# Kernel optimization log

Hardware: AMD Instinct MI355X
Metric: run time of the kernel (lower is better)

The kernel has to match this reference:

```python
import jax, jax.numpy as jnp
import numpy as np

# dims
B, T, E = 2, 4096, 512
H = 8
DH = E // H            # 64 per-head dim
DEPTH = 4
NHASH = 4              # n_hashes
BUCKET = 64            # bucket_size
NB = T // BUCKET       # n_buckets = 64 (even)
VOCAB, NCLASS = 32000, 10
FF = 4 * E
MASK_VAL = -1e9        # causal mask value
SELF_VAL = -5e4        # TOKEN_SELF_ATTN_VALUE


def layer_norm(x, g, b):
    m = jnp.mean(x, axis=-1, keepdims=True)
    v = jnp.var(x, axis=-1, keepdims=True)
    return (x - m) * jax.lax.rsqrt(v + 1e-5) * g + b


def lsh_attention(x, wqk, wv, wo, bo, rot):
    """Reformer LSH causal self-attention (eval mode, shared QK, n_hashes rounds)."""
    qk = (x @ wqk).reshape(B, T, H, DH).transpose(0, 2, 1, 3).reshape(B * H, T, DH)
    v = (x @ wv).reshape(B, T, H, DH).transpose(0, 2, 1, 3).reshape(B * H, T, DH)
    b = B * H
    # --- hash: random rotations -> bucket ids per hash round ---
    rotated = jnp.einsum('btf,fhi->bhti', qk, rot)             # (b, NHASH, T, NB//2)
    rotated = jnp.concatenate([rotated, -rotated], axis=-1)    # (b, NHASH, T, NB)
    buckets = jnp.argmax(rotated, axis=-1)                     # (b, NHASH, T)
    buckets = buckets + (jnp.arange(NHASH) * NB)[None, :, None]
    buckets = buckets.reshape(b, NHASH * T)
    # --- stable sort by (bucket, time) ---
    ticker = jnp.arange(NHASH * T)
    bt = buckets * T + (ticker % T)
    sticker = jnp.argsort(bt, axis=-1)                         # sort permutation
    undo_sort = jnp.argsort(sticker, axis=-1)
    st = sticker % T                                           # original time index of sorted slot
    sqk = jnp.take_along_axis(qk, st[..., None], axis=1)
    sv = jnp.take_along_axis(v, st[..., None], axis=1)
    # --- chunk into buckets, attend to own + previous chunk ---
    C = NHASH * NB                                             # number of chunks
    bq_t = st.reshape(b, C, BUCKET)
    bqk = sqk.reshape(b, C, BUCKET, DH)
    bv = sv.reshape(b, C, BUCKET, DH)
    bq = bqk
    bk = bqk / jnp.maximum(jnp.linalg.norm(bqk, axis=-1, keepdims=True), 1e-12)
    look = lambda t: jnp.concatenate([t, jnp.roll(t, 1, axis=1)], axis=2)
    bk, bvl, bkv_t = look(bk), look(bv), look(bq_t)
    dots = jnp.einsum('bcie,bcje->bcij', bq, bk) * (DH ** -0.5)  # (b, C, BUCKET, 2*BUCKET)
    causal = bq_t[:, :, :, None] < bkv_t[:, :, None, :]
    dots = jnp.where(causal, MASK_VAL, dots)
    self_m = bq_t[:, :, :, None] == bkv_t[:, :, None, :]
    dots = jnp.where(self_m, SELF_VAL, dots)
    lse = jax.nn.logsumexp(dots, axis=-1, keepdims=True)
    probs = jnp.exp(dots - lse)
    so = jnp.einsum('bcij,bcje->bcie', probs, bvl).reshape(b, NHASH * T, DH)
    slogits = lse.reshape(b, NHASH * T)
    # --- unsort and combine hash rounds via logsumexp weights ---
    o = jnp.take_along_axis(so, undo_sort[..., None], axis=1).reshape(b, NHASH, T, DH)
    logits = jnp.take_along_axis(slogits, undo_sort, axis=1).reshape(b, NHASH, T, 1)
    w = jnp.exp(logits - jax.nn.logsumexp(logits, axis=1, keepdims=True))
    out = jnp.sum(o * w, axis=1)                               # (b, T, DH)
    out = out.reshape(B, H, T, DH).transpose(0, 2, 1, 3).reshape(B, T, E)
    return out @ wo + bo


def feed_forward(x, w1, b1, w2, b2):
    return jax.nn.gelu(x @ w1 + b1, approximate=False) @ w2 + b2


def setup_inputs() -> dict:
    key = jax.random.key(0)
    ks = jax.random.split(key, 12)
    n = lambda k, s: (0.02 * jax.random.normal(k, s)).astype(jnp.float32)
    return {
        'x': jax.random.randint(ks[0], (B, T), 0, VOCAB),
        'tok_emb': n(ks[1], (VOCAB, E)),
        'pos_emb': n(ks[2], (T, E)),
        'rotations': jax.random.normal(ks[3], (DEPTH, DH, NHASH, NB // 2), dtype=jnp.float32),
        'ln1_g': jnp.ones((DEPTH, E), jnp.float32), 'ln1_b': jnp.zeros((DEPTH, E), jnp.float32),
        'w_qk': n(ks[4], (DEPTH, E, E)), 'w_v': n(ks[5], (DEPTH, E, E)),
        'w_o': n(ks[6], (DEPTH, E, E)), 'b_o': jnp.zeros((DEPTH, E), jnp.float32),
        'ln2_g': jnp.ones((DEPTH, E), jnp.float32), 'ln2_b': jnp.zeros((DEPTH, E), jnp.float32),
        'w_ff1': n(ks[7], (DEPTH, E, FF)), 'b_ff1': jnp.zeros((DEPTH, FF), jnp.float32),
        'w_ff2': n(ks[8], (DEPTH, FF, E)), 'b_ff2': jnp.zeros((DEPTH, E), jnp.float32),
        'w_final': n(ks[9], (E, NCLASS)), 'b_final': jnp.zeros((NCLASS,), jnp.float32),
    }


def reference(x, tok_emb, pos_emb, rotations, ln1_g, ln1_b, w_qk, w_v, w_o, b_o,
              ln2_g, ln2_b, w_ff1, b_ff1, w_ff2, b_ff2, w_final, b_final):
    h = tok_emb[x] + pos_emb[None, :, :]
    # reversible sequence: y1 = x1 + attn(ln(x2)); y2 = x2 + ff(ln(y1))
    x1, x2 = h, h
    for d in range(DEPTH):
        x1 = x1 + lsh_attention(layer_norm(x2, ln1_g[d], ln1_b[d]),
                                w_qk[d], w_v[d], w_o[d], b_o[d], rotations[d])
        x2 = x2 + feed_forward(layer_norm(x1, ln2_g[d], ln2_b[d]),
                               w_ff1[d], b_ff1[d], w_ff2[d], b_ff2[d])
    h = 0.5 * (x1 + x2)
    pooled = jnp.mean(h, axis=1)          # pooling == 'avg'
    return pooled @ w_final + b_final
```

## Files before the change

### kernel.cpp

```cpp
#include <hip/hip_runtime.h>
#include <hip/hip_bf16.h>
#include <math.h>

#define B_      2
#define T_      4096
#define E_      512
#define H_      8
#define DH_     64
#define DEPTH_  4
#define NHASH_  4
#define BUCKET_ 64
#define NB_     64
#define NB2_    32
#define C_      (NHASH_*NB_)
#define BH_     (B_*H_)
#define NT_     (NHASH_*T_)
#define FF_     2048
#define NCLASS_ 10
#define MASKV   (-1e9f)
#define SELFV   (-5e4f)

typedef __attribute__((ext_vector_type(8))) short short8;
typedef __attribute__((ext_vector_type(4))) float f32x4;

__device__ __forceinline__ void gload_lds16(const void* g, void* l) {
    __builtin_amdgcn_global_load_lds(
        (const __attribute__((address_space(1))) void*)g,
        (__attribute__((address_space(3))) void*)l,
        16, 0, 0);
}

__device__ __forceinline__ unsigned pk2(float a, float b) {
    __hip_bfloat16 ha = __float2bfloat16(a), hb = __float2bfloat16(b);
    unsigned short ua = *(unsigned short*)&ha, ub = *(unsigned short*)&hb;
    return (unsigned)ua | ((unsigned)ub << 16);
}

__global__ __launch_bounds__(128) void k_embed(const int* __restrict__ x, const float* __restrict__ tok,
                                               const float* __restrict__ pos, float* __restrict__ x1,
                                               float* __restrict__ x2)
{
    int bt = blockIdx.x;
    int t  = bt & (T_ - 1);
    int id = x[bt];
    float4 tv = ((const float4*)(tok + (size_t)id * E_))[threadIdx.x];
    float4 pv = ((const float4*)(pos + (size_t)t * E_))[threadIdx.x];
    float4 hv = make_float4(tv.x + pv.x, tv.y + pv.y, tv.z + pv.z, tv.w + pv.w);
    ((float4*)(x1 + (size_t)bt * E_))[threadIdx.x] = hv;
    ((float4*)(x2 + (size_t)bt * E_))[threadIdx.x] = hv;
}

template<bool LO>
__global__ __launch_bounds__(128) void k_ln(const float* __restrict__ in, const float* __restrict__ g,
                                            const float* __restrict__ b, __hip_bfloat16* __restrict__ out,
                                            __hip_bfloat16* __restrict__ outlo)
{
    int row = blockIdx.x, tid = threadIdx.x;
    float4 v = ((const float4*)(in + (size_t)row * E_))[tid];
    float s = v.x + v.y + v.z + v.w;
    float q = v.x * v.x + v.y * v.y + v.z * v.z + v.w * v.w;
#pragma unroll
    for (int d = 1; d < 64; d <<= 1) { s += __shfl_xor(s, d); q += __shfl_xor(q, d); }
    __shared__ float red[4];
    int w = tid >> 6;
    if ((tid & 63) == 0) { red[w * 2] = s; red[w * 2 + 1] = q; }
    __syncthreads();
    s = red[0] + red[2]; q = red[1] + red[3];
    float mean = s * (1.0f / E_);
    float var  = q * (1.0f / E_) - mean * mean;
    float rstd = rsqrtf(var + 1e-5f);
    float4 gv = ((const float4*)g)[tid];
    float4 bv = ((const float4*)b)[tid];
    float o0 = (v.x - mean) * rstd * gv.x + bv.x;
    float o1 = (v.y - mean) * rstd * gv.y + bv.y;
    float o2 = (v.z - mean) * rstd * gv.z + bv.z;
    float o3 = (v.w - mean) * rstd * gv.w + bv.w;
    __hip_bfloat16* op = out + (size_t)row * E_ + tid * 4;
    __hip_bfloat16 h0 = __float2bfloat16(o0), h1 = __float2bfloat16(o1);
    __hip_bfloat16 h2 = __float2bfloat16(o2), h3 = __float2bfloat16(o3);
    op[0] = h0; op[1] = h1; op[2] = h2; op[3] = h3;
    if (LO) {
        __hip_bfloat16* lp = outlo + (size_t)row * E_ + tid * 4;
        lp[0] = __float2bfloat16(o0 - __bfloat162float(h0));
        lp[1] = __float2bfloat16(o1 - __bfloat162float(h1));
        lp[2] = __float2bfloat16(o2 - __bfloat162float(h2));
        lp[3] = __float2bfloat16(o3 - __bfloat162float(h3));
    }
}

template<bool SPLIT>
__global__ __launch_bounds__(256) void k_wprep(const float* __restrict__ W, __hip_bfloat16* __restrict__ WT,
                                               __hip_bfloat16* __restrict__ WTlo, int K, int N)
{
    __shared__ float tile[32][33];
    int n0 = blockIdx.x * 32, k0 = blockIdx.y * 32;
    int tx = threadIdx.x & 31, ty = threadIdx.x >> 5;
#pragma unroll
    for (int i = 0; i < 4; ++i) {
        int k = ty + i * 8;
        tile[k][tx] = W[(size_t)(k0 + k) * N + n0 + tx];
    }
    __syncthreads();
#pragma unroll
    for (int i = 0; i < 4; ++i) {
        int n = ty + i * 8;
        float v = tile[tx][n];
        __hip_bfloat16 hv = __float2bfloat16(v);
        WT[(size_t)(n0 + n) * K + k0 + tx] = hv;
        if (SPLIT)
            WTlo[(size_t)(n0 + n) * K + k0 + tx] = __float2bfloat16(v - __bfloat162float(hv));
    }
}

__global__ __launch_bounds__(256) void k_rotprep(const float* __restrict__ rot,
                                                 __hip_bfloat16* __restrict__ rhs,
                                                 __hip_bfloat16* __restrict__ rls)
{
    int tid = threadIdx.x;
    for (int idx = tid; idx < 128 * 64; idx += 256) {
        int row = idx >> 6, f = idx & 63;
        float v = rot[(size_t)f * 128 + row];
        __hip_bfloat16 hv = __float2bfloat16(v);
        __hip_bfloat16 lv = __float2bfloat16(v - __bfloat162float(hv));
        int b = f >> 3;
        int off = row * 64 + (((b ^ (row & 7)) << 3) | (f & 7));
        rhs[off] = hv;
        rls[off] = lv;
    }
}

__device__ __forceinline__ float geluf(float xx) {
    return 0.5f * xx * (1.0f + erff(xx * 0.70710678118654752f));
}

template<int OUTK, int BIAS, int TM>
__global__ __launch_bounds__(256) void k_mgemm(const __hip_bfloat16* __restrict__ A,
                                               const __hip_bfloat16* __restrict__ WT,
                                               const float* __restrict__ bias, void* __restrict__ Cout,
                                               int N, int K, int nbnShift)
{
    constexpr int MF = TM / 32;
    constexpr int ABUF = TM * 64;
    __shared__ __align__(16) char smem[32768];
    char* AbBase = smem;
    char* BbBase = smem + 2 * ABUF;

    int tid = threadIdx.x;
    int lane = tid & 63, w = tid >> 6;
    int nwg = gridDim.x;
    int bid = blockIdx.x;
    int swz = (bid & 7) * (nwg >> 3) + (bid >> 3);
    int nmask = (1 << nbnShift) - 1;
    int m0 = (swz >> nbnShift) * TM, n0 = (swz & nmask) * 128;
    int wm = (w >> 1) * (TM / 2), wn = (w & 1) * 64;

    int r0 = tid >> 2, s0 = tid & 3;
    int c0 = (s0 - (r0 >> 1)) & 3;
    int r1 = r0 + 64;
    int c1 = (s0 - (r1 >> 1)) & 3;
    const __hip_bfloat16* aS0 = A  + (size_t)(m0 + r0) * K + c0 * 8;
    const __hip_bfloat16* aS1 = A  + (size_t)(m0 + r1) * K + c1 * 8;
    const __hip_bfloat16* bS0 = WT + (size_t)(n0 + r0) * K + c0 * 8;
    const __hip_bfloat16* bS1 = WT + (size_t)(n0 + r1) * K + c1 * 8;

    int cch = lane >> 4;
    int aoff[MF], boff[4];
#pragma unroll
    for (int f = 0; f < MF; ++f) {
        int ar = wm + f * 16 + (lane & 15);
        aoff[f] = ar * 32 + (((cch + (ar >> 1)) & 3) * 8);
    }
#pragma unroll
    for (int f = 0; f < 4; ++f) {
        int br = wn + f * 16 + (lane & 15);
        boff[f] = br * 32 + (((cch + (br >> 1)) & 3) * 8);
    }

    f32x4 acc[MF][4];
#pragma unroll
    for (int i = 0; i < MF; ++i)
#pragma unroll
        for (int j = 0; j < 4; ++j) acc[i][j] = (f32x4){0.f, 0.f, 0.f, 0.f};

    const int NS = K >> 5;
    {
        gload_lds16(aS0, AbBase + tid * 16);
        if constexpr (TM == 128) gload_lds16(aS1, AbBase + 4096 + tid * 16);
        gload_lds16(bS0, BbBase + tid * 16);
        gload_lds16(bS1, BbBase + 4096 + tid * 16);
    }
    __syncthreads();
    for (int s = 0; s < NS; ++s) {
        int cur = s & 1;
        if (s + 1 < NS) {
            int nb = cur ^ 1;
            int kk = (s + 1) * 32;
            char* Abn = AbBase + nb * ABUF;
            char* Bbn = BbBase + nb * 8192;
            gload_lds16(aS0 + kk, Abn + tid * 16);
            if constexpr (TM == 128) gload_lds16(aS1 + kk, Abn + 4096 + tid * 16);
            gload_lds16(bS0 + kk, Bbn + tid * 16);
            gload_lds16(bS1 + kk, Bbn + 4096 + tid * 16);
        }
        const __hip_bfloat16* Ab = (const __hip_bfloat16*)(AbBase + cur * ABUF);
        const __hip_bfloat16* Bb = (const __hip_bfloat16*)(BbBase + cur * 8192);
        short8 af[MF], bfr[4];
#pragma unroll
        for (int f = 0; f < MF; ++f) af[f] = *(const short8*)(Ab + aoff[f]);
#pragma unroll
        for (int f = 0; f < 4; ++f)  bfr[f] = *(const short8*)(Bb + boff[f]);
#pragma unroll
        for (int i = 0; i < MF; ++i)
#pragma unroll
            for (int j = 0; j < 4; ++j)
                acc[i][j] = __builtin_amdgcn_mfma_f32_16x16x32_bf16(af[i], bfr[j], acc[i][j], 0, 0, 0);
        __syncthreads();
    }

    int g = lane >> 4;
    if (OUTK == 2 || OUTK == 3) {
        unsigned short* Ot = (unsigned short*)smem;
#pragma unroll
        for (int i = 0; i < MF; ++i) {
#pragma unroll
            for (int j = 0; j < 4; ++j) {
                int col = wn + j * 16 + (lane & 15);
                float bv = BIAS ? bias[n0 + col] : 0.f;
#pragma unroll
                for (int q = 0; q < 4; ++q) {
                    int row = wm + i * 16 + g * 4 + q;
                    float vv = acc[i][j][q] + bv;
                    if (OUTK == 2) vv = geluf(vv);
                    __hip_bfloat16 hv = __float2bfloat16(vv);
                    Ot[row * 128 + (((col >> 3) ^ (row & 7)) << 3) + (col & 7)] = *(unsigned short*)&hv;
                }
            }
        }
        __syncthreads();
#pragma unroll
        for (int u = 0; u < TM / 16; ++u) {
            int f = u * 256 + tid;
            int row = f >> 4, cblk = f & 15;
            uint4 v = *(const uint4*)(Ot + row * 128 + ((cblk ^ (row & 7)) << 3));
            if (OUTK == 2) {
                *(uint4*)((__hip_bfloat16*)Cout + (size_t)(m0 + row) * N + n0 + cblk * 8) = v;
            } else {
                int mrow = m0 + row;
                int t = mrow & (T_ - 1), bI = mrow >> 12;
                int col = n0 + cblk * 8;
                int h = col >> 6, fin = col & 63;
                *(uint4*)((__hip_bfloat16*)Cout + ((size_t)(bI * H_ + h) * T_ + t) * 64 + fin) = v;
            }
        }
    } else if (TM == 64) {
        float* Ot = (float*)smem;
        float* Cb = (float*)Cout;
#pragma unroll
        for (int i = 0; i < MF; ++i) {
#pragma unroll
            for (int j = 0; j < 4; ++j) {
                int col = wn + j * 16 + (lane & 15);
#pragma unroll
                for (int q = 0; q < 4; ++q) {
                    int row = wm + i * 16 + g * 4 + q;
                    Ot[row * 128 + (((col >> 2) ^ (row & 7)) << 2) + (col & 3)] = acc[i][j][q];
                }
            }
        }
        __syncthreads();
#pragma unroll
        for (int u = 0; u < 8; ++u) {
            int f = u * 256 + tid;
            int row = f >> 5, c4 = f & 31;
            float4 v = *(const float4*)(Ot + row * 128 + ((c4 ^ (row & 7)) << 2));
            if (BIAS) {
                float4 bv = *(const float4*)(bias + n0 + c4 * 4);
                v.x += bv.x; v.y += bv.y; v.z += bv.z; v.w += bv.w;
            }
            float* cp = Cb + (size_t)(m0 + row) * N + n0 + c4 * 4;
            float4 old = *(const float4*)cp;
            v.x += old.x; v.y += old.y; v.z += old.z; v.w += old.w;
            *(float4*)cp = v;
        }
    } else {
        float* Ot = (float*)smem;
        float* Cb = (float*)Cout;
#pragma unroll
        for (int half = 0; half < 2; ++half) {
            if ((w >> 1) == half) {
#pragma unroll
                for (int i = 0; i < MF; ++i) {
#pragma unroll
                    for (int j = 0; j < 4; ++j) {
                        int col = wn + j * 16 + (lane & 15);
#pragma unroll
                        for (int q = 0; q < 4; ++q) {
                            int rowl = i * 16 + g * 4 + q;
                            Ot[rowl * 128 + (((col >> 2) ^ (rowl & 7)) << 2) + (col & 3)] = acc[i][j][q];
                        }
                    }
                }
            }
            __syncthreads();
#pragma unroll
            for (int u = 0; u < 8; ++u) {
                int f = u * 256 + tid;
                int row = f >> 5, c4 = f & 31;
                float4 v = *(const float4*)(Ot + row * 128 + ((c4 ^ (row & 7)) << 2));
                if (BIAS) {
                    float4 bv = *(const float4*)(bias + n0 + c4 * 4);
                    v.x += bv.x; v.y += bv.y; v.z += bv.z; v.w += bv.w;
                }
                float* cp = Cb + (size_t)(m0 + half * 64 + row) * N + n0 + c4 * 4;
                float4 old = *(const float4*)cp;
                v.x += old.x; v.y += old.y; v.z += old.z; v.w += old.w;
                *(float4*)cp = v;
            }
            __syncthreads();
        }
    }
}

__global__ __launch_bounds__(256) void k_mgemm_qk(const __hip_bfloat16* __restrict__ Ah,
                                                  const __hip_bfloat16* __restrict__ Al,
                                                  const __hip_bfloat16* __restrict__ Bh,
                                                  const __hip_bfloat16* __restrict__ Bl,
                                                  float* __restrict__ Cout)
{
    __shared__ __align__(16) char smem[49152];
    const int N = 512, K = 512;
    int tid = threadIdx.x;
    int lane = tid & 63, w = tid >> 6;
    int nwg = gridDim.x;
    int bid = blockIdx.x;
    int swz = (bid & 7) * (nwg >> 3) + (bid >> 3);
    int m0 = (swz >> 2) * 64, n0 = (swz & 3) * 128;
    int wm = (w >> 1) * 32, wn = (w & 1) * 64;

    int r0 = tid >> 2, s0 = tid & 3;
    int c0 = (s0 - (r0 >> 1)) & 3;
    int r1 = r0 + 64;
    int c1 = (s0 - (r1 >> 1)) & 3;
    const __hip_bfloat16* ahS  = Ah + (size_t)(m0 + r0) * K + c0 * 8;
    const __hip_bfloat16* alS  = Al + (size_t)(m0 + r0) * K + c0 * 8;
    const __hip_bfloat16* bhS0 = Bh + (size_t)(n0 + r0) * K + c0 * 8;
    const __hip_bfloat16* bhS1 = Bh + (size_t)(n0 + r1) * K + c1 * 8;
    const __hip_bfloat16* blS0 = Bl + (size_t)(n0 + r0) * K + c0 * 8;
    const __hip_bfloat16* blS1 = Bl + (size_t)(n0 + r1) * K + c1 * 8;

    int cch = lane >> 4;
    int aoff[2], boff[4];
#pragma unroll
    for (int f = 0; f < 2; ++f) {
        int ar = wm + f * 16 + (lane & 15);
        aoff[f] = ar * 32 + (((cch + (ar >> 1)) & 3) * 8);
    }
#pragma unroll
    for (int f = 0; f < 4; ++f) {
        int br = wn + f * 16 + (lane & 15);
        boff[f] = br * 32 + (((cch + (br >> 1)) & 3) * 8);
    }

    f32x4 acc[2][4];
#pragma unroll
    for (int i = 0; i < 2; ++i)
#pragma unroll
        for (int j = 0; j < 4; ++j) acc[i][j] = (f32x4){0.f, 0.f, 0.f, 0.f};

#define QK_STAGE(buf, kk)                                                     \
    { char* bb = smem + (buf) * 24576;                                        \
      gload_lds16(ahS  + (kk), bb + tid * 16);                                \
      gload_lds16(alS  + (kk), bb + 4096  + tid * 16);                        \
      gload_lds16(bhS0 + (kk), bb + 8192  + tid * 16);                        \
      gload_lds16(bhS1 + (kk), bb + 12288 + tid * 16);                        \
      gload_lds16(blS0 + (kk), bb + 16384 + tid * 16);                        \
      gload_lds16(blS1 + (kk), bb + 20480 + tid * 16); }

    QK_STAGE(0, 0)
    __syncthreads();
    const int NS = K >> 5;
    for (int s = 0; s < NS; ++s) {
        int cur = s & 1;
        if (s + 1 < NS) QK_STAGE(cur ^ 1, (s + 1) * 32)
        const __hip_bfloat16* AhB = (const __hip_bfloat16*)(smem + cur * 24576);
        const __hip_bfloat16* AlB = (const __hip_bfloat16*)(smem + cur * 24576 + 4096);
        const __hip_bfloat16* BhB = (const __hip_bfloat16*)(smem + cur * 24576 + 8192);
        const __hip_bfloat16* BlB = (const __hip_bfloat16*)(smem + cur * 24576 + 16384);
        short8 afh[2], afl[2], bfh[4], bfl[4];
#pragma unroll
        for (int f = 0; f < 2; ++f) {
            afh[f] = *(const short8*)(AhB + aoff[f]);
            afl[f] = *(const short8*)(AlB + aoff[f]);
        }
#pragma unroll
        for (int f = 0; f < 4; ++f) {
            bfh[f] = *(const short8*)(BhB + boff[f]);
            bfl[f] = *(const short8*)(BlB + boff[f]);
        }
#pragma unroll
        for (int i = 0; i < 2; ++i)
#pragma unroll
            for (int j = 0; j < 4; ++j) {
                acc[i][j] = __builtin_amdgcn_mfma_f32_16x16x32_bf16(afh[i], bfh[j], acc[i][j], 0, 0, 0);
                acc[i][j] = __builtin_amdgcn_mfma_f32_16x16x32_bf16(afh[i], bfl[j], acc[i][j], 0, 0, 0);
                acc[i][j] = __builtin_amdgcn_mfma_f32_16x16x32_bf16(afl[i], bfh[j], acc[i][j], 0, 0, 0);
            }
        __syncthreads();
    }
#undef QK_STAGE

    int g = lane >> 4;
    float* Ot = (float*)smem;
#pragma unroll
    for (int i = 0; i < 2; ++i) {
#pragma unroll
        for (int j = 0; j < 4; ++j) {
            int col = wn + j * 16 + (lane & 15);
#pragma unroll
            for (int q = 0; q < 4; ++q) {
                int row = wm + i * 16 + g * 4 + q;
                Ot[row * 128 + (((col >> 2) ^ (row & 7)) << 2) + (col & 3)] = acc[i][j][q];
            }
        }
    }
    __syncthreads();
#pragma unroll
    for (int u = 0; u < 8; ++u) {
        int f = u * 256 + tid;
        int row = f >> 5, c4 = f & 31;
        float4 v = *(const float4*)(Ot + row * 128 + ((c4 ^ (row & 7)) << 2));
        *(float4*)(Cout + (size_t)(m0 + row) * N + n0 + c4 * 4) = v;
    }
}

__global__ __launch_bounds__(256) void k_hash(const float* __restrict__ qk,
                                              const __hip_bfloat16* __restrict__ rhs,
                                              const __hip_bfloat16* __restrict__ rls,
                                              unsigned char* __restrict__ bkt,
                                              __hip_bfloat16* __restrict__ qh,
                                              __hip_bfloat16* __restrict__ kh)
{
    __shared__ __align__(16) char smem[65536];
    char* RH = smem;
    char* RL = smem + 16384;
    char* QH = smem + 32768;
    char* QL = smem + 49152;
    int tid = threadIdx.x, lane = tid & 63, wv = tid >> 6;
    int bh = blockIdx.x, tc = blockIdx.y;
    int bI = bh >> 3, h = bh & 7;

#pragma unroll
    for (int it = 0; it < 4; ++it) {
        gload_lds16((const char*)rhs + it * 4096 + tid * 16, RH + it * 4096 + tid * 16);
        gload_lds16((const char*)rls + it * 4096 + tid * 16, RL + it * 4096 + tid * 16);
    }

    {
        int t = tid >> 1, half = tid & 1;
        int tg = tc * 128 + t;
        const float4* qsrc = (const float4*)(qk + ((size_t)(bI * T_ + tg)) * E_ + h * DH_ + half * 32);
        float4 q4[8];
        float n2 = 0.f;
#pragma unroll
        for (int j = 0; j < 8; ++j) {
            q4[j] = qsrc[j];
            n2 += q4[j].x * q4[j].x + q4[j].y * q4[j].y + q4[j].z * q4[j].z + q4[j].w * q4[j].w;
        }
        n2 += __shfl_xor(n2, 1);
        float sc = 0.125f / fmaxf(sqrtf(n2), 1e-12f);
        float qv[32];
#pragma unroll
        for (int j = 0; j < 8; ++j) {
            qv[4 * j] = q4[j].x; qv[4 * j + 1] = q4[j].y; qv[4 * j + 2] = q4[j].z; qv[4 * j + 3] = q4[j].w;
        }
        unsigned short hb[32], lb[32], kb[32];
#pragma unroll
        for (int j = 0; j < 32; ++j) {
            __hip_bfloat16 hv = __float2bfloat16(qv[j]);
            __hip_bfloat16 lv = __float2bfloat16(qv[j] - __bfloat162float(hv));
            __hip_bfloat16 kv = __float2bfloat16(qv[j] * sc);
            hb[j] = *(unsigned short*)&hv; lb[j] = *(unsigned short*)&lv; kb[j] = *(unsigned short*)&kv;
        }
        size_t ro = ((size_t)bh * T_ + tg) * 64 + half * 32;
        uint4* qdst = (uint4*)(qh + ro);
        uint4* kdst = (uint4*)(kh + ro);
#pragma unroll
        for (int j = 0; j < 4; ++j) {
            qdst[j] = *(uint4*)&hb[8 * j];
            kdst[j] = *(uint4*)&kb[8 * j];
        }
#pragma unroll
        for (int j = 0; j < 4; ++j) {
            int b = half * 4 + j;
            int xo = t * 128 + ((b ^ (t & 7)) << 4);
            *(uint4*)(QH + xo) = *(uint4*)&hb[8 * j];
            *(uint4*)(QL + xo) = *(uint4*)&lb[8 * j];
        }
    }
    __syncthreads();

#pragma unroll
    for (int sub = 0; sub < 2; ++sub) {
        int tl = wv * 32 + sub * 16 + (lane & 15);
        int g = lane >> 4;
        short8 qfh0 = *(const short8*)(QH + tl * 128 + ((g ^ (tl & 7)) << 4));
        short8 qfh1 = *(const short8*)(QH + tl * 128 + (((4 + g) ^ (tl & 7)) << 4));
        short8 qfl0 = *(const short8*)(QL + tl * 128 + ((g ^ (tl & 7)) << 4));
        short8 qfl1 = *(const short8*)(QL + tl * 128 + (((4 + g) ^ (tl & 7)) << 4));
        f32x4 sacc[8];
#pragma unroll
        for (int kt = 0; kt < 8; ++kt) sacc[kt] = (f32x4){0.f, 0.f, 0.f, 0.f};
#pragma unroll
        for (int kt = 0; kt < 8; ++kt) {
            int row = kt * 16 + (lane & 15);
            short8 rh0 = *(const short8*)(RH + row * 128 + ((g ^ (row & 7)) << 4));
            short8 rh1 = *(const short8*)(RH + row * 128 + (((4 + g) ^ (row & 7)) << 4));
            short8 rl0 = *(const short8*)(RL + row * 128 + ((g ^ (row & 7)) << 4));
            short8 rl1 = *(const short8*)(RL + row * 128 + (((4 + g) ^ (row & 7)) << 4));
            sacc[kt] = __builtin_amdgcn_mfma_f32_16x16x32_bf16(rh0, qfh0, sacc[kt], 0, 0, 0);
            sacc[kt] = __builtin_amdgcn_mfma_f32_16x16x32_bf16(rh1, qfh1, sacc[kt], 0, 0, 0);
            sacc[kt] = __builtin_amdgcn_mfma_f32_16x16x32_bf16(rl0, qfh0, sacc[kt], 0, 0, 0);
            sacc[kt] = __builtin_amdgcn_mfma_f32_16x16x32_bf16(rl1, qfh1, sacc[kt], 0, 0, 0);
            sacc[kt] = __builtin_amdgcn_mfma_f32_16x16x32_bf16(rh0, qfl0, sacc[kt], 0, 0, 0);
            sacc[kt] = __builtin_amdgcn_mfma_f32_16x16x32_bf16(rh1, qfl1, sacc[kt], 0, 0, 0);
        }
#pragma unroll
        for (int rd = 0; rd < 4; ++rd) {
            float bv = -3.0e38f; int bi = 0;
#pragma unroll
            for (int kp = 0; kp < 2; ++kp) {
#pragma unroll
                for (int rr = 0; rr < 4; ++rr) {
                    int i = kp * 16 + g * 4 + rr;
                    float v = sacc[rd * 2 + kp][rr];
                    if (v > bv) { bv = v; bi = i; }
                }
            }
#pragma unroll
            for (int kp = 0; kp < 2; ++kp) {
#pragma unroll
                for (int rr = 0; rr < 4; ++rr) {
                    int i = 32 + kp * 16 + g * 4 + rr;
                    float v = -sacc[rd * 2 + kp][rr];
                    if (v > bv) { bv = v; bi = i; }
                }
            }
#pragma unroll
            for (int dlt = 16; dlt <= 32; dlt <<= 1) {
                float ov = __shfl_xor(bv, dlt);
                int oi = __shfl_xor(bi, dlt);
                if (ov > bv || (ov == bv && oi < bi)) { bv = ov; bi = oi; }
            }
            if (g == 0)
                bkt[((size_t)(bh * NHASH_ + rd)) * T_ + tc * 128 + tl] = (unsigned char)bi;
        }
    }
}

__global__ __launch_bounds__(64) void k_sort(const unsigned char* __restrict__ bkt, int* __restrict__ st)
{
    __shared__ unsigned char bktL[T_];
    __shared__ int hist[64][65];
    __shared__ int goff[NB_];
    int tid = threadIdx.x;
    int bhr = blockIdx.x;
    const unsigned char* src = bkt + (size_t)bhr * T_;
#pragma unroll
    for (int i = 0; i < 4; ++i)
        ((uint4*)bktL)[tid * 4 + i] = ((const uint4*)src)[tid * 4 + i];
#pragma unroll
    for (int j = 0; j < 16; ++j) ((int4*)&hist[tid][0])[j] = make_int4(0, 0, 0, 0);
    int base = tid * 64;
#pragma unroll 8
    for (int i = 0; i < 64; ++i) hist[tid][bktL[base + i]]++;
    __syncthreads();
    int run = 0;
#pragma unroll 8
    for (int s = 0; s < 64; ++s) { int v = hist[s][tid]; hist[s][tid] = run; run += v; }
    int tot = run;
    int pre = tot;
#pragma unroll
    for (int d = 1; d < 64; d <<= 1) { int o = __shfl_up(pre, d); if (tid >= d) pre += o; }
    goff[tid] = pre - tot;
    __syncthreads();
#pragma unroll 8
    for (int b = 0; b < 64; ++b) hist[tid][b] += goff[b];
    int* dst = st + (size_t)bhr * T_;
#pragma unroll 8
    for (int i = 0; i < 64; ++i) {
        int b = bktL[base + i];
        int off = hist[tid][b]++;
        dst[off] = base + i;
    }
}

__global__ __launch_bounds__(256, 2) void k_attn(const __hip_bfloat16* __restrict__ qh,
                                                 const __hip_bfloat16* __restrict__ kh,
                                                 const __hip_bfloat16* __restrict__ vh,
                                                 const int* __restrict__ st,
                                                 __hip_bfloat16* __restrict__ o,
                                                 float* __restrict__ lg)
{
    __shared__ __align__(16) char smem[49664];
    char* KbB = smem;
    char* VtB = smem + 16384;
    char* PbB = smem + 32768;
    int*  kvt = (int*)(smem + 49152);
    unsigned short* ObU = (unsigned short*)smem;

    int tid = threadIdx.x;
    int lane = tid & 63;
    int g = lane >> 4;
    int wv = tid >> 6;
    int wq0 = wv * 16;

    int bid = blockIdx.x;
    int bh = ((bid & 7) << 1) | ((bid >> 3) & 1);
    int c  = bid >> 4;
    int rnd = c >> 6;
    int cp = (c + C_ - 1) & (C_ - 1);
    const size_t stB = (size_t)bh * NT_;

    if (tid < 128) {
        int cc = (tid < 64) ? c : cp;
        kvt[tid] = st[stB + (size_t)cc * 64 + (tid & 63)];
    }
    __syncthreads();

    {
        int k = tid >> 1, half = tid & 1;
        const uint4* src = (const uint4*)(kh + ((size_t)bh * T_ + kvt[k]) * 64 + half * 32);
#pragma unroll
        for (int j2 = 0; j2 < 4; ++j2) {
            uint4 a = src[j2];
            int blk = (half * 4 + j2) ^ (k & 7);
            *(uint4*)(KbB + k * 128 + blk * 16) = a;
        }
    }
    {
        int kp = tid & 63, dq = tid >> 6;
        const uint4* r0 = (const uint4*)(vh + ((size_t)bh * T_ + kvt[2 * kp]) * 64 + dq * 16);
        const uint4* r1 = (const uint4*)(vh + ((size_t)bh * T_ + kvt[2 * kp + 1]) * 64 + dq * 16);
        unsigned short va[16], vb2[16];
        *(uint4*)&va[0] = r0[0];  *(uint4*)&va[8] = r0[1];
        *(uint4*)&vb2[0] = r1[0]; *(uint4*)&vb2[8] = r1[1];
#pragma unroll
        for (int i = 0; i < 16; ++i) {
            int d = dq * 16 + i;
            unsigned wrd = (unsigned)va[i] | ((unsigned)vb2[i] << 16);
            *(unsigned*)(VtB + d * 256 + ((((kp >> 2) ^ i)) << 4) + ((kp & 3) << 2)) = wrd;
        }
    }
    int tq = kvt[wq0 + (lane & 15)];
    const __hip_bfloat16* qrow = qh + ((size_t)bh * T_ + tq) * 64;
    short8 qf0 = *(const short8*)(qrow + g * 8);
    short8 qf1 = *(const short8*)(qrow + 32 + g * 8);
    __syncthreads();

    f32x4 sacc[8];
#pragma unroll
    for (int kt = 0; kt < 8; ++kt) sacc[kt] = (f32x4){0.f, 0.f, 0.f, 0.f};
#pragma unroll
    for (int kt = 0; kt < 8; ++kt) {
        int row = kt * 16 + (lane & 15);
        short8 kf0 = *(const short8*)(KbB + row * 128 + (((g) ^ (row & 7)) << 4));
        short8 kf1 = *(const short8*)(KbB + row * 128 + (((4 + g) ^ (row & 7)) << 4));
        sacc[kt] = __builtin_amdgcn_mfma_f32_16x16x32_bf16(kf0, qf0, sacc[kt], 0, 0, 0);
        sacc[kt] = __builtin_amdgcn_mfma_f32_16x16x32_bf16(kf1, qf1, sacc[kt], 0, 0, 0);
    }

    float m = -3.0e38f;
#pragma unroll
    for (int kt = 0; kt < 8; ++kt) {
#pragma unroll
        for (int r = 0; r < 4; ++r) {
            int tk = kvt[kt * 16 + g * 4 + r];
            float dd = sacc[kt][r];
            dd = (tk > tq) ? MASKV : dd;
            dd = (tk == tq) ? SELFV : dd;
            sacc[kt][r] = dd;
            m = fmaxf(m, dd);
        }
    }
    m = fmaxf(m, __shfl_xor(m, 16));
    m = fmaxf(m, __shfl_xor(m, 32));
    float ssum = 0.f;
#pragma unroll
    for (int kt = 0; kt < 8; ++kt) {
        float p0 = __expf(sacc[kt][0] - m);
        float p1 = __expf(sacc[kt][1] - m);
        float p2 = __expf(sacc[kt][2] - m);
        float p3 = __expf(sacc[kt][3] - m);
        ssum += (p0 + p1) + (p2 + p3);
        uint2 wrd = make_uint2(pk2(p0, p1), pk2(p2, p3));
        int blk = (kt * 2 + (g >> 1)) ^ (lane & 15);
        *(uint2*)(PbB + (wq0 + (lane & 15)) * 256 + (blk << 4) + ((g & 1) << 3)) = wrd;
    }
    ssum += __shfl_xor(ssum, 16);
    ssum += __shfl_xor(ssum, 32);
    if (lane < 16)
        lg[stB + (size_t)rnd * T_ + tq] = m + __logf(ssum);

    f32x4 pacc[4];
#pragma unroll
    for (int dt = 0; dt < 4; ++dt) pacc[dt] = (f32x4){0.f, 0.f, 0.f, 0.f};
#pragma unroll
    for (int s = 0; s < 4; ++s) {
        int xr = ((s * 4 + g) ^ (lane & 15)) << 4;
        short8 pf = *(const short8*)(PbB + (wq0 + (lane & 15)) * 256 + xr);
#pragma unroll
        for (int dt = 0; dt < 4; ++dt) {
            short8 vf = *(const short8*)(VtB + (dt * 16 + (lane & 15)) * 256 + xr);
            pacc[dt] = __builtin_amdgcn_mfma_f32_16x16x32_bf16(pf, vf, pacc[dt], 0, 0, 0);
        }
    }
    __syncthreads();

#pragma unroll
    for (int r = 0; r < 4; ++r) {
        float sr = __shfl(ssum, g * 4 + r);
        float inv = 1.0f / sr;
        int rowl = wq0 + g * 4 + r;
#pragma unroll
        for (int dt = 0; dt < 4; ++dt) {
            __hip_bfloat16 hv = __float2bfloat16(pacc[dt][r] * inv);
            ObU[rowl * 72 + dt * 16 + (lane & 15)] = *(unsigned short*)&hv;
        }
    }
    __syncthreads();

    {
        int rr = tid >> 2, seg = tid & 3;
        uint4 a = *(const uint4*)(ObU + rr * 72 + seg * 16);
        uint4 b = *(const uint4*)(ObU + rr * 72 + seg * 16 + 8);
        size_t jor = stB + (size_t)rnd * T_ + kvt[rr];
        uint4* dst = (uint4*)(o + jor * 64 + seg * 16);
        dst[0] = a; dst[1] = b;
    }
}

__global__ __launch_bounds__(256) void k_combine(const __hip_bfloat16* __restrict__ o,
                                                 const float* __restrict__ lg,
                                                 __hip_bfloat16* __restrict__ att)
{
    int bt = blockIdx.x;
    int bI = bt >> 12;
    int t  = bt & (T_ - 1);
    for (int e = threadIdx.x; e < E_; e += 256) {
        int h = e >> 6, f = e & 63;
        size_t base = ((size_t)(bI * H_ + h)) * NT_ + t;
        float L0 = lg[base], L1 = lg[base + T_], L2 = lg[base + 2 * T_], L3 = lg[base + 3 * T_];
        float M = fmaxf(fmaxf(L0, L1), fmaxf(L2, L3));
        float w0 = __expf(L0 - M), w1 = __expf(L1 - M), w2 = __expf(L2 - M), w3 = __expf(L3 - M);
        float sw = w0 + w1 + w2 + w3;
        float val = __bfloat162float(o[base * DH_ + f]) * w0
                  + __bfloat162float(o[(base + T_) * DH_ + f]) * w1
                  + __bfloat162float(o[(base + 2 * T_) * DH_ + f]) * w2
                  + __bfloat162float(o[(base + 3 * T_) * DH_ + f]) * w3;
        att[(size_t)bt * E_ + e] = __float2bfloat16(val / sw);
    }
}

__global__ __launch_bounds__(256) void k_pool1(const float* __restrict__ x1, const float* __restrict__ x2,
                                               float* __restrict__ part)
{
    int blk = blockIdx.x;
    int bI = blk >> 5, tc = blk & 31;
    int t0 = tc * 128;
    for (int e = threadIdx.x; e < E_; e += 256) {
        float s = 0.f;
        for (int t = t0; t < t0 + 128; ++t) {
            size_t idx = ((size_t)bI * T_ + t) * E_ + e;
            s += x1[idx] + x2[idx];
        }
        part[((size_t)bI * 32 + tc) * E_ + e] = s;
    }
}

__global__ __launch_bounds__(256) void k_final(const float* __restrict__ part, const float* __restrict__ wf,
                                               const float* __restrict__ bf, float* __restrict__ out)
{
    __shared__ float pooled[B_ * E_];
    int tid = threadIdx.x;
    for (int i = tid; i < B_ * E_; i += 256) {
        int bI = i >> 9, e = i & 511;
        float s = 0.f;
        for (int c2 = 0; c2 < 32; ++c2) s += part[((size_t)bI * 32 + c2) * E_ + e];
        pooled[i] = s * (0.5f / T_);
    }
    __syncthreads();
    if (tid < B_ * NCLASS_) {
        int bI = tid / NCLASS_, cl = tid % NCLASS_;
        float s = bf[cl];
        for (int e = 0; e < E_; ++e) s += pooled[bI * E_ + e] * wf[(size_t)e * NCLASS_ + cl];
        out[tid] = s;
    }
}

extern "C" void kernel_launch(void* const* d_in, const int* in_sizes, int n_in,
                              void* d_out, int out_size, void* d_ws, size_t ws_size,
                              hipStream_t stream)
{
    const int*   X    = (const int*)d_in[0];
    const float* TOK  = (const float*)d_in[1];
    const float* POS  = (const float*)d_in[2];
    const float* ROT  = (const float*)d_in[3];
    const float* LN1G = (const float*)d_in[4];
    const float* LN1B = (const float*)d_in[5];
    const float* WQK  = (const float*)d_in[6];
    const float* WV   = (const float*)d_in[7];
    const float* WO   = (const float*)d_in[8];
    const float* BO   = (const float*)d_in[9];
    const float* LN2G = (const float*)d_in[10];
    const float* LN2B = (const float*)d_in[11];
    const float* WF1  = (const float*)d_in[12];
    const float* BF1  = (const float*)d_in[13];
    const float* WF2  = (const float*)d_in[14];
    const float* BF2  = (const float*)d_in[15];
    const float* WFIN = (const float*)d_in[16];
    const float* BFIN = (const float*)d_in[17];

    float* ws = (float*)d_ws;
    const size_t S = (size_t)B_ * T_ * E_;
    float* x1   = ws;
    float* x2   = x1 + S;
    float* qkb  = x2 + S;
    float* vb   = qkb + S;
    float* bigf = vb + S;
    float* lgb  = bigf + 2 * S;
    float* part = lgb + (size_t)BH_ * NT_;
    __hip_bfloat16* lnbh  = (__hip_bfloat16*)(part + (size_t)B_ * 32 * E_);
    __hip_bfloat16* lnbl  = lnbh + S;
    __hip_bfloat16* attnb = lnbl + S;
    int*   stb  = (int*)(attnb + S);
    __hip_bfloat16* WTbase = (__hip_bfloat16*)(stb + (size_t)BH_ * NT_);
    __hip_bfloat16* big    = (__hip_bfloat16*)bigf;

    const size_t W55 = (size_t)512 * 512;
    const size_t WFF = (size_t)2048 * 512;
    __hip_bfloat16* WTqk_hi = WTbase;
    __hip_bfloat16* WTqk_lo = WTqk_hi + 4 * W55;
    __hip_bfloat16* WTv     = WTqk_lo + 4 * W55;
    __hip_bfloat16* WTo     = WTv     + 4 * W55;
    __hip_bfloat16* WTf1    = WTo     + 4 * W55;
    __hip_bfloat16* WTf2    = WTf1    + 4 * WFF;
    unsigned char*  bktb    = (unsigned char*)(WTf2 + 4 * WFF);
    __hip_bfloat16* qh      = (__hip_bfloat16*)(bktb + (size_t)BH_ * NHASH_ * T_);
    __hip_bfloat16* khb     = qh  + (size_t)BH_ * T_ * 64;
    __hip_bfloat16* vhb     = khb + (size_t)BH_ * T_ * 64;
    __hip_bfloat16* rswzh   = vhb + (size_t)BH_ * T_ * 64;
    __hip_bfloat16* rswzl   = rswzh + 4 * 8192;

    for (int d = 0; d < DEPTH_; ++d) {
        k_wprep<true ><<<dim3(16, 16), 256, 0, stream>>>(WQK + d * W55, WTqk_hi + d * W55,
                                                         WTqk_lo + d * W55, 512, 512);
        k_wprep<false><<<dim3(16, 16), 256, 0, stream>>>(WV + d * W55, WTv + d * W55, nullptr, 512, 512);
        k_wprep<false><<<dim3(16, 16), 256, 0, stream>>>(WO + d * W55, WTo + d * W55, nullptr, 512, 512);
        k_wprep<false><<<dim3(64, 16), 256, 0, stream>>>(WF1 + d * WFF, WTf1 + d * WFF, nullptr, 512, 2048);
        k_wprep<false><<<dim3(16, 64), 256, 0, stream>>>(WF2 + d * WFF, WTf2 + d * WFF, nullptr, 2048, 512);
        k_rotprep<<<1, 256, 0, stream>>>(ROT + (size_t)d * 64 * 128, rswzh + d * 8192, rswzl + d * 8192);
    }

    const int g512_64 = (512 / 128) * ((B_ * T_) / 64);
    const int gff     = (FF_ / 128) * ((B_ * T_) / 128);

    k_embed<<<B_ * T_, 128, 0, stream>>>(X, TOK, POS, x1, x2);
    for (int d = 0; d < DEPTH_; ++d) {
        k_ln<true><<<B_ * T_, 128, 0, stream>>>(x2, LN1G + (size_t)d * E_, LN1B + (size_t)d * E_, lnbh, lnbl);
        k_mgemm_qk<<<g512_64, 256, 0, stream>>>(lnbh, lnbl, WTqk_hi + d * W55, WTqk_lo + d * W55, qkb);
        k_mgemm<3, 0, 64><<<g512_64, 256, 0, stream>>>(lnbh, WTv + d * W55, nullptr, vhb, 512, 512, 2);
        k_hash<<<dim3(BH_, T_ / 128), 256, 0, stream>>>(qkb, rswzh + d * 8192, rswzl + d * 8192,
                                                        bktb, qh, khb);
        k_sort<<<BH_ * NHASH_, 64, 0, stream>>>(bktb, stb);
        k_attn<<<BH_ * C_, 256, 0, stream>>>(qh, khb, vhb, stb, big, lgb);
        k_combine<<<B_ * T_, 256, 0, stream>>>(big, lgb, attnb);
        k_mgemm<1, 1, 64><<<g512_64, 256, 0, stream>>>(attnb, WTo + d * W55, BO + (size_t)d * E_, x1,
                                                       512, 512, 2);
        k_ln<false><<<B_ * T_, 128, 0, stream>>>(x1, LN2G + (size_t)d * E_, LN2B + (size_t)d * E_, lnbh, nullptr);
        k_mgemm<2, 1, 128><<<gff, 256, 0, stream>>>(lnbh, WTf1 + d * WFF, BF1 + (size_t)d * FF_, big,
                                                    2048, 512, 4);
        k_mgemm<1, 1, 64><<<g512_64, 256, 0, stream>>>(big, WTf2 + d * WFF, BF2 + (size_t)d * E_, x2,
                                                       512, 2048, 2);
    }
    k_pool1<<<B_ * 32, 256, 0, stream>>>(x1, x2, part);
    k_final<<<1, 256, 0, stream>>>(part, WFIN, BFIN, (float*)d_out);
}
```

Baseline: 879.3 us.

## Add 256x256 pipelined GELU GEMM for FF1 and enlarge other GEMM M-tiles

Adds a new 512-thread GEMM kernel with 256x256 output tiles, 128KB LDS double buffering, direct global-to-LDS loads interleaved with four MFMA phases, and a fused bias+GELU epilogue that writes bf16 through swizzled LDS. The first feed-forward GEMM uses it in place of the 128-tile generic kernel. The V, output-projection and FF2 GEMMs switch from 64-row to 128-row M tiles with half the grid. The aim is more operand reuse per tile and less global traffic, at the cost of fewer workgroups, more register pressure, and occupancy capped by LDS use.

```diff
diff --git a/kernel.cpp b/kernel.cpp
--- a/kernel.cpp
+++ b/kernel.cpp
@@ -321,6 +321,132 @@
     }
 }
 
+#define STG_A(buf, kt, h) \
+    gload_lds16(aSrc + (size_t)((h) * 128) * K + (kt) * 64,      smem + (buf) * 32768 + (h) * 16384 + tid * 16); \
+    gload_lds16(aSrc + (size_t)((h) * 128 + 64) * K + (kt) * 64, smem + (buf) * 32768 + (h) * 16384 + 8192 + tid * 16);
+#define STG_B(buf, kt, h) \
+    gload_lds16(bSrc + (size_t)((h) * 128) * K + (kt) * 64,      smem + 65536 + (buf) * 32768 + (h) * 16384 + tid * 16); \
+    gload_lds16(bSrc + (size_t)((h) * 128 + 64) * K + (kt) * 64, smem + 65536 + (buf) * 32768 + (h) * 16384 + 8192 + tid * 16);
+
+#define PHASE8(buf, MH, NH, STAGE, GATE) do {                                                     \
+    const char* Ab_ = smem + (buf) * 32768;                                                       \
+    const char* Bb_ = smem + 65536 + (buf) * 32768;                                               \
+    short8 aF[4][2], bF[2][2];                                                                    \
+    _Pragma("unroll")                                                                             \
+    for (int mf = 0; mf < 4; ++mf) {                                                              \
+        int row = arow + (MH) * 128 + mf * 16;                                                    \
+        aF[mf][0] = *(const short8*)(Ab_ + row * 128 + sw0);                                      \
+        aF[mf][1] = *(const short8*)(Ab_ + row * 128 + sw1);                                      \
+    }                                                                                             \
+    _Pragma("unroll")                                                                             \
+    for (int nf = 0; nf < 2; ++nf) {                                                              \
+        int row = brow + (NH) * 128 + nf * 16;                                                    \
+        bF[nf][0] = *(const short8*)(Bb_ + row * 128 + sw0);                                      \
+        bF[nf][1] = *(const short8*)(Bb_ + row * 128 + sw1);                                      \
+    }                                                                                             \
+    STAGE                                                                                         \
+    GATE                                                                                          \
+    __builtin_amdgcn_s_barrier();                                                                 \
+    asm volatile("s_waitcnt lgkmcnt(0)" ::: "memory");                                            \
+    __builtin_amdgcn_sched_barrier(0);                                                            \
+    __builtin_amdgcn_s_setprio(1);                                                                \
+    _Pragma("unroll")                                                                             \
+    for (int mf = 0; mf < 4; ++mf)                                                                \
+        _Pragma("unroll")                                                                         \
+        for (int nf = 0; nf < 2; ++nf) {                                                          \
+            acc[MH][NH][mf][nf] = __builtin_amdgcn_mfma_f32_16x16x32_bf16(aF[mf][0], bF[nf][0], acc[MH][NH][mf][nf], 0, 0, 0); \
+            acc[MH][NH][mf][nf] = __builtin_amdgcn_mfma_f32_16x16x32_bf16(aF[mf][1], bF[nf][1], acc[MH][NH][mf][nf], 0, 0, 0); \
+        }                                                                                         \
+    __builtin_amdgcn_s_setprio(0);                                                                \
+    __builtin_amdgcn_s_barrier();                                                                 \
+} while (0)
+
+__global__ __launch_bounds__(512, 2) void k_gemm256_gelu(const __hip_bfloat16* __restrict__ A,
+                                                         const __hip_bfloat16* __restrict__ WT,
+                                                         const float* __restrict__ bias,
+                                                         __hip_bfloat16* __restrict__ Cout,
+                                                         int N, int K, int nShift)
+{
+    __shared__ __align__(16) char smem[131072];
+    const int NT = K >> 6;
+    int tid = threadIdx.x;
+    int lane = tid & 63, w = tid >> 6;
+    int lane7 = lane & 7, cch = lane >> 4;
+    int nwg = gridDim.x;
+    int bid = blockIdx.x;
+    int swz = (bid & 7) * (nwg >> 3) + (bid >> 3);
+    int m0 = (swz >> nShift) * 256;
+    int n0 = (swz & ((1 << nShift) - 1)) * 256;
+
+    int rstg = tid >> 3;
+    int kcstg = (tid & 7) ^ (rstg & 7);
+    const __hip_bfloat16* aSrc = A  + (size_t)(m0 + rstg) * K + kcstg * 8;
+    const __hip_bfloat16* bSrc = WT + (size_t)(n0 + rstg) * K + kcstg * 8;
+
+    int arow = (w >> 2) * 64 + (lane & 15);
+    int brow = (w & 3) * 32 + (lane & 15);
+    int sw0 = (cch ^ lane7) << 4;
+    int sw1 = ((4 + cch) ^ lane7) << 4;
+
+    f32x4 acc[2][2][4][2];
+#pragma unroll
+    for (int a2 = 0; a2 < 2; ++a2)
+#pragma unroll
+        for (int b2 = 0; b2 < 2; ++b2)
+#pragma unroll
+            for (int c2 = 0; c2 < 4; ++c2)
+#pragma unroll
+                for (int d2 = 0; d2 < 2; ++d2) acc[a2][b2][c2][d2] = (f32x4){0.f, 0.f, 0.f, 0.f};
+
+    STG_A(0, 0, 0) STG_A(0, 0, 1) STG_B(0, 0, 0) STG_B(0, 0, 1)
+    if (NT > 1) { STG_A(1, 1, 0) STG_B(1, 1, 1) }
+    if (NT > 1) asm volatile("s_waitcnt vmcnt(4)" ::: "memory");
+    else        asm volatile("s_waitcnt vmcnt(0)" ::: "memory");
+    __builtin_amdgcn_s_barrier();
+
+    for (int t = 0; t < NT; ++t) {
+        int buf = t & 1;
+        PHASE8(buf, 0, 0, { if (t + 1 < NT) { STG_A(buf ^ 1, t + 1, 1) } }, {});
+        PHASE8(buf, 0, 1, { if (t + 1 < NT) { STG_B(buf ^ 1, t + 1, 0) } }, {});
+        PHASE8(buf, 1, 1, { if (t + 2 < NT) { STG_A(buf, t + 2, 0) } }, {});
+        PHASE8(buf, 1, 0, { if (t + 2 < NT) { STG_B(buf, t + 2, 1) } },
+               { if (t + 2 < NT)      asm volatile("s_waitcnt vmcnt(4)" ::: "memory");
+                 else if (t + 1 < NT) asm volatile("s_waitcnt vmcnt(0)" ::: "memory"); });
+    }
+
+    unsigned short* Ot = (unsigned short*)smem;
+    int g = lane >> 4;
+#pragma unroll
+    for (int mh = 0; mh < 2; ++mh)
+#pragma unroll
+        for (int nh = 0; nh < 2; ++nh)
+#pragma unroll
+            for (int nf = 0; nf < 2; ++nf) {
+                int coll = nh * 128 + (w & 3) * 32 + nf * 16 + (lane & 15);
+                float bv = bias[n0 + coll];
+#pragma unroll
+                for (int mf = 0; mf < 4; ++mf)
+#pragma unroll
+                    for (int q = 0; q < 4; ++q) {
+                        int rowl = mh * 128 + (w >> 2) * 64 + mf * 16 + g * 4 + q;
+                        float vv = geluf(acc[mh][nh][mf][nf][q] + bv);
+                        __hip_bfloat16 hv = __float2bfloat16(vv);
+                        Ot[rowl * 256 + ((((coll >> 4) ^ (rowl & 7)) << 4) | (coll & 15))] = *(unsigned short*)&hv;
+                    }
+            }
+    __syncthreads();
+#pragma unroll
+    for (int u = 0; u < 16; ++u) {
+        int f = u * 512 + tid;
+        int rowl = f >> 5, c16 = f & 31;
+        uint4 v = *(const uint4*)(Ot + rowl * 256 + ((((c16 >> 1) ^ (rowl & 7)) << 4) | ((c16 & 1) << 3)));
+        *(uint4*)(Cout + (size_t)(m0 + rowl) * N + n0 + c16 * 8) = v;
+    }
+}
+#undef PHASE8
+#undef STG_A
+#undef STG_B
+
 __global__ __launch_bounds__(256) void k_mgemm_qk(const __hip_bfloat16* __restrict__ Ah,
                                                   const __hip_bfloat16* __restrict__ Al,
                                                   const __hip_bfloat16* __restrict__ Bh,
@@ -861,26 +987,27 @@
         k_rotprep<<<1, 256, 0, stream>>>(ROT + (size_t)d * 64 * 128, rswzh + d * 8192, rswzl + d * 8192);
     }
 
-    const int g512_64 = (512 / 128) * ((B_ * T_) / 64);
-    const int gff     = (FF_ / 128) * ((B_ * T_) / 128);
+    const int g512_64  = (512 / 128) * ((B_ * T_) / 64);
+    const int g512_128 = (512 / 128) * ((B_ * T_) / 128);
+    const int gff1     = ((B_ * T_) / 256) * (FF_ / 256);
 
     k_embed<<<B_ * T_, 128, 0, stream>>>(X, TOK, POS, x1, x2);
     for (int d = 0; d < DEPTH_; ++d) {
         k_ln<true><<<B_ * T_, 128, 0, stream>>>(x2, LN1G + (size_t)d * E_, LN1B + (size_t)d * E_, lnbh, lnbl);
         k_mgemm_qk<<<g512_64, 256, 0, stream>>>(lnbh, lnbl, WTqk_hi + d * W55, WTqk_lo + d * W55, qkb);
-        k_mgemm<3, 0, 64><<<g512_64, 256, 0, stream>>>(lnbh, WTv + d * W55, nullptr, vhb, 512, 512, 2);
+        k_mgemm<3, 0, 128><<<g512_128, 256, 0, stream>>>(lnbh, WTv + d * W55, nullptr, vhb, 512, 512, 2);
         k_hash<<<dim3(BH_, T_ / 128), 256, 0, stream>>>(qkb, rswzh + d * 8192, rswzl + d * 8192,
                                                         bktb, qh, khb);
         k_sort<<<BH_ * NHASH_, 64, 0, stream>>>(bktb, stb);
         k_attn<<<BH_ * C_, 256, 0, stream>>>(qh, khb, vhb, stb, big, lgb);
         k_combine<<<B_ * T_, 256, 0, stream>>>(big, lgb, attnb);
-        k_mgemm<1, 1, 64><<<g512_64, 256, 0, stream>>>(attnb, WTo + d * W55, BO + (size_t)d * E_, x1,
-                                                       512, 512, 2);
+        k_mgemm<1, 1, 128><<<g512_128, 256, 0, stream>>>(attnb, WTo + d * W55, BO + (size_t)d * E_, x1,
+                                                         512, 512, 2);
         k_ln<false><<<B_ * T_, 128, 0, stream>>>(x1, LN2G + (size_t)d * E_, LN2B + (size_t)d * E_, lnbh, nullptr);
-        k_mgemm<2, 1, 128><<<gff, 256, 0, stream>>>(lnbh, WTf1 + d * WFF, BF1 + (size_t)d * FF_, big,
-                                                    2048, 512, 4);
-        k_mgemm<1, 1, 64><<<g512_64, 256, 0, stream>>>(big, WTf2 + d * WFF, BF2 + (size_t)d * E_, x2,
-                                                       512, 2048, 2);
+        k_gemm256_gelu<<<gff1, 512, 0, stream>>>(lnbh, WTf1 + d * WFF, BF1 + (size_t)d * FF_, big,
+                                                 2048, 512, 3);
+        k_mgemm<1, 1, 128><<<g512_128, 256, 0, stream>>>(big, WTf2 + d * WFF, BF2 + (size_t)d * E_, x2,
+                                                         512, 2048, 2);
     }
     k_pool1<<<B_ * 32, 256, 0, stream>>>(x1, x2, part);
     k_final<<<1, 256, 0, stream>>>(part, WFIN, BFIN, (float*)d_out);
```

New measurement: 950.7 us. 8.1% more time.
